# Kernel tuning notes

Measured on AMD Instinct MI355X. Metric: run time of the kernel, lower is better.

## Reference

```python
import jax, jax.numpy as jnp
import numpy as np

D_MODEL = 2048
N_HEADS = 32
N_KV_HEADS = 8
D_K = D_MODEL // N_HEADS          # 64
N_REP = N_HEADS // N_KV_HEADS     # 4
KV_DIM = N_KV_HEADS * D_K         # 512
B, T = 4, 2048


def setup_inputs() -> dict:
    key = jax.random.key(0)
    ks = jax.random.split(key, 9)
    s_in = 1.0 / np.sqrt(D_MODEL)
    x = jax.random.normal(ks[0], (B, T, D_MODEL), dtype=jnp.float32)
    Wq = jax.random.uniform(ks[1], (D_MODEL, D_MODEL), jnp.float32, -s_in, s_in)
    bq = jax.random.uniform(ks[2], (D_MODEL,), jnp.float32, -s_in, s_in)
    Wk = jax.random.uniform(ks[3], (D_MODEL, KV_DIM), jnp.float32, -s_in, s_in)
    bk = jax.random.uniform(ks[4], (KV_DIM,), jnp.float32, -s_in, s_in)
    Wv = jax.random.uniform(ks[5], (D_MODEL, KV_DIM), jnp.float32, -s_in, s_in)
    bv = jax.random.uniform(ks[6], (KV_DIM,), jnp.float32, -s_in, s_in)
    Wo = jax.random.uniform(ks[7], (D_MODEL, D_MODEL), jnp.float32, -s_in, s_in)
    bo = jax.random.uniform(ks[8], (D_MODEL,), jnp.float32, -s_in, s_in)
    return {"x": x, "Wq": Wq, "bq": bq, "Wk": Wk, "bk": bk,
            "Wv": Wv, "bv": bv, "Wo": Wo, "bo": bo}


def reference(x, Wq, bq, Wk, bk, Wv, bv, Wo, bo):
    Bsz, S, _ = x.shape
    # projections
    q = x @ Wq + bq                                   # (B, T, d_model)
    k = x @ Wk + bk                                   # (B, T, kv_dim)
    v = x @ Wv + bv
    # (B, n_kv, n_rep, T, d_k) for q; (B, n_kv, T, d_k) for k, v.
    # Grouping q by kv head avoids materializing repeated K/V.
    q = q.reshape(Bsz, S, N_KV_HEADS, N_REP, D_K).transpose(0, 2, 3, 1, 4)
    k = k.reshape(Bsz, S, N_KV_HEADS, D_K).transpose(0, 2, 1, 3)
    v = v.reshape(Bsz, S, N_KV_HEADS, D_K).transpose(0, 2, 1, 3)
    scale = 1.0 / np.sqrt(D_K).astype(np.float32)
    scores = jnp.einsum('bgrtd,bgsd->bgrts', q, k) * scale  # (B, n_kv, n_rep, T, T)
    causal = jnp.tril(jnp.ones((S, S), dtype=bool))
    scores = jnp.where(causal, scores, jnp.finfo(scores.dtype).min)
    p = jax.nn.softmax(scores, axis=-1)
    o = jnp.einsum('bgrts,bgsd->bgrtd', p, v)               # (B, n_kv, n_rep, T, d_k)
    o = o.transpose(0, 3, 1, 2, 4).reshape(Bsz, S, D_MODEL)
    return o @ Wo + bo
```

## Files before the change

kernel.cpp:

```cpp
#include <hip/hip_runtime.h>
#include <cstdint>
#include <cstddef>

typedef __attribute__((ext_vector_type(8))) short short8;
typedef __attribute__((ext_vector_type(4))) float f32x4;

#define D_MODEL 2048
#define KV_DIM  512
#define N_HEADS 32
#define N_KV    8
#define D_K     64
#define B_SZ    4
#define T_SEQ   2048
#define M_TOT   (B_SZ * T_SEQ)
#define N1      (D_MODEL + 2 * KV_DIM)
#define NEG_BIG (-1e30f)

__device__ __forceinline__ unsigned short f2bf(float f) {
    union { float f; unsigned int i; } c; c.f = f;
    unsigned int u = c.i;
    u += 0x7FFFu + ((u >> 16) & 1u);
    return (unsigned short)(u >> 16);
}

__device__ __forceinline__ unsigned int cvtpk_bf16(float lo, float hi) {
    unsigned int r;
    asm("v_cvt_pk_bf16_f32 %0, %1, %2" : "=v"(r) : "v"(lo), "v"(hi));
    return r;
}

__device__ __forceinline__ void async16(unsigned short* lds, const unsigned short* g) {
    __builtin_amdgcn_global_load_lds(
        (const __attribute__((address_space(1))) unsigned int*)g,
        (__attribute__((address_space(3))) unsigned int*)lds, 16, 0, 0);
}

__global__ __launch_bounds__(256)
void stage_x(const float* __restrict__ x, unsigned short* __restrict__ xb, int n) {
    for (int i = blockIdx.x * blockDim.x + threadIdx.x; i * 4 < n;
         i += gridDim.x * blockDim.x) {
        const f32x4 v = *(const f32x4*)&x[i * 4];
        unsigned short o[4];
#pragma unroll
        for (int k = 0; k < 4; k++) o[k] = f2bf(v[k]);
        *(uint64_t*)&xb[i * 4] = *(const uint64_t*)o;
    }
}

__global__ __launch_bounds__(256)
void transpose_f32_bf16(const float* __restrict__ src,
                        unsigned short* __restrict__ dst, int R, int C) {
    __shared__ unsigned short tile[32][34];
    int bx = blockIdx.x * 32;
    int by = blockIdx.y * 32;
    int tx = threadIdx.x;
    int ty = threadIdx.y;
#pragma unroll
    for (int i = 0; i < 32; i += 8)
        tile[ty + i][tx] = f2bf(src[(size_t)(by + ty + i) * C + bx + tx]);
    __syncthreads();
#pragma unroll
    for (int i = 0; i < 32; i += 8)
        dst[(size_t)(bx + ty + i) * R + by + tx] = tile[tx][ty + i];
}

template <int MODE>
__global__ __launch_bounds__(256)
void gemm_bt(const unsigned short* __restrict__ A,
             const unsigned short* __restrict__ Bt,
             const float* __restrict__ b0,
             const float* __restrict__ b1,
             const float* __restrict__ b2,
             unsigned short* __restrict__ out0,
             unsigned short* __restrict__ out1,
             unsigned short* __restrict__ out2,
             float* __restrict__ outF,
             int K) {
    __shared__ __align__(16) unsigned short As[128 * 32];
    __shared__ __align__(16) unsigned short Bs[128 * 32];

    const int t    = threadIdx.x;
    const int wave = t >> 6;
    const int lane = t & 63;
    const int quad = lane >> 4;
    const int l16  = lane & 15;
    const int wm   = (wave >> 1) * 64;
    const int wn   = (wave & 1) * 64;
    const int rowBase = blockIdx.y * 128;
    const int colBase = blockIdx.x * 128;

    f32x4 acc[4][4];
#pragma unroll
    for (int i = 0; i < 4; i++)
#pragma unroll
        for (int j = 0; j < 4; j++)
            acc[i][j] = (f32x4){0.f, 0.f, 0.f, 0.f};

    const int r0  = t >> 2;
    const int off = (t & 3) * 8;
    const unsigned short* Ap = A  + (size_t)(rowBase + r0) * K + off;
    const unsigned short* Bp = Bt + (size_t)(colBase + r0) * K + off;
    const size_t rowStep = (size_t)64 * K;

    for (int k0 = 0; k0 < K; k0 += 32) {
        *(short8*)&As[t * 8]         = *(const short8*)(Ap + k0);
        *(short8*)&As[(t + 256) * 8] = *(const short8*)(Ap + rowStep + k0);
        *(short8*)&Bs[t * 8]         = *(const short8*)(Bp + k0);
        *(short8*)&Bs[(t + 256) * 8] = *(const short8*)(Bp + rowStep + k0);
        __syncthreads();

        short8 af[4], bfr[4];
#pragma unroll
        for (int i = 0; i < 4; i++)
            af[i] = *(const short8*)&As[(wm + i * 16 + l16) * 32 + quad * 8];
#pragma unroll
        for (int i = 0; i < 4; i++)
            bfr[i] = *(const short8*)&Bs[(wn + i * 16 + l16) * 32 + quad * 8];

#pragma unroll
        for (int mi = 0; mi < 4; mi++)
#pragma unroll
            for (int ni = 0; ni < 4; ni++)
                acc[mi][ni] = __builtin_amdgcn_mfma_f32_16x16x32_bf16(
                    af[mi], bfr[ni], acc[mi][ni], 0, 0, 0);
        __syncthreads();
    }

#pragma unroll
    for (int mi = 0; mi < 4; mi++) {
        const int rowT = rowBase + wm + mi * 16 + quad * 4;
#pragma unroll
        for (int ni = 0; ni < 4; ni++) {
            const int col = colBase + wn + ni * 16 + l16;
#pragma unroll
            for (int r = 0; r < 4; r++) {
                float v = acc[mi][ni][r];
                const int rr = rowT + r;
                if (MODE == 0) {
                    if (col < D_MODEL) {
                        v += b0[col];
                        out0[(size_t)rr * D_MODEL + col] = f2bf(v);
                    } else if (col < D_MODEL + KV_DIM) {
                        const int c = col - D_MODEL;
                        v += b1[c];
                        out1[(size_t)rr * KV_DIM + c] = f2bf(v);
                    } else {
                        const int c = col - (D_MODEL + KV_DIM);
                        v += b2[c];
                        const int b   = rr >> 11;
                        const int tt  = rr & 2047;
                        const int kvh = c >> 6;
                        const int d   = c & 63;
                        out2[((size_t)((b * N_KV + kvh) * D_K + d)) * T_SEQ + tt] = f2bf(v);
                    }
                } else {
                    v += b0[col];
                    outF[(size_t)rr * D_MODEL + col] = v;
                }
            }
        }
    }
}

__global__ __launch_bounds__(256)
void attn_fwd(const unsigned short* __restrict__ qb,
              const unsigned short* __restrict__ kb,
              const unsigned short* __restrict__ vt,
              unsigned short* __restrict__ ob) {
    __shared__ __align__(16) unsigned short Ks[2][64 * 64];
    __shared__ __align__(16) unsigned short Vs[2][64 * 64];

    const int t    = threadIdx.x;
    const int wave = t >> 6;
    const int lane = t & 63;
    const int quad = lane >> 4;
    const int l16  = lane & 15;
    const int qt   = (int)gridDim.x - 1 - (int)blockIdx.x;
    const int h    = blockIdx.y;
    const int b    = blockIdx.z;
    const int kvh  = h >> 2;
    const int qBase = qt * 128;
    const int rowG  = b * T_SEQ;
    const size_t vtBase = (size_t)(b * N_KV + kvh) * D_K * T_SEQ;

    short8 qf[2][2];
#pragma unroll
    for (int mi = 0; mi < 2; mi++) {
        const int row = rowG + qBase + wave * 32 + mi * 16 + l16;
#pragma unroll
        for (int kk = 0; kk < 2; kk++)
            qf[mi][kk] = *(const short8*)&qb[(size_t)row * D_MODEL + h * D_K + kk * 32 + quad * 8];
    }

    f32x4 oacc[2][4];
#pragma unroll
    for (int i = 0; i < 2; i++)
#pragma unroll
        for (int j = 0; j < 4; j++)
            oacc[i][j] = (f32x4){0.f, 0.f, 0.f, 0.f};
    float m_run[2], l_run[2];
#pragma unroll
    for (int i = 0; i < 2; i++) { m_run[i] = NEG_BIG; l_run[i] = 0.f; }

    const int rr  = t >> 3;
    const int sc8 = ((t & 7) ^ (rr & 7)) << 3;

    auto stage = [&](int bi, int sB) {
#pragma unroll
        for (int i = 0; i < 2; i++) {
            const int row = i * 32 + rr;
            async16(&Ks[bi][(i * 32 + wave * 8) * 64],
                    kb + (size_t)(rowG + sB + row) * KV_DIM + kvh * D_K + sc8);
            async16(&Vs[bi][(i * 32 + wave * 8) * 64],
                    vt + vtBase + (size_t)row * T_SEQ + sB + sc8);
        }
    };

    const float scale = 0.125f;
    const int jMax = 2 * qt + 1;
    int buf = 0;

    stage(0, 0);
    __syncthreads();

    for (int j = 0; j <= jMax; ++j) {
        if (j < jMax) stage(buf ^ 1, (j + 1) * 64);

        if (!(j == jMax && wave < 2)) {
            const int sBase = j * 64;
            const bool diag = (j >= 2 * qt);
            const int sRel  = sBase - qBase;
            const char* KsB = (const char*)&Ks[buf][0];
            const char* VsB = (const char*)&Vs[buf][0];
            const int swz   = (l16 & 7) << 4;

            f32x4 sacc[4][2];
            __builtin_amdgcn_s_setprio(1);
#pragma unroll
            for (int ni = 0; ni < 4; ni++) {
                const int rowB = (ni * 16 + l16) * 128;
                const short8 kf0 = *(const short8*)(KsB + rowB + ((quad * 16) ^ swz));
                const short8 kf1 = *(const short8*)(KsB + rowB + ((64 + quad * 16) ^ swz));
#pragma unroll
                for (int mi = 0; mi < 2; mi++) {
                    f32x4 s = (f32x4){0.f, 0.f, 0.f, 0.f};
                    s = __builtin_amdgcn_mfma_f32_16x16x32_bf16(kf0, qf[mi][0], s, 0, 0, 0);
                    s = __builtin_amdgcn_mfma_f32_16x16x32_bf16(kf1, qf[mi][1], s, 0, 0, 0);
                    sacc[ni][mi] = s;
                }
            }
            __builtin_amdgcn_s_setprio(0);

            uint2 packed[4][2];
#pragma unroll
            for (int mi = 0; mi < 2; mi++) {
                float tm = NEG_BIG;
#pragma unroll
                for (int ni = 0; ni < 4; ni++)
#pragma unroll
                    for (int r = 0; r < 4; r++) {
                        float v = sacc[ni][mi][r] * scale;
                        if (diag) {
                            const int kc = sRel + ni * 16 + quad * 4 + r;
                            const int qr = wave * 32 + mi * 16 + l16;
                            if (kc > qr) v = NEG_BIG;
                        }
                        sacc[ni][mi][r] = v;
                        tm = fmaxf(tm, v);
                    }
                tm = fmaxf(tm, __shfl_xor(tm, 16));
                tm = fmaxf(tm, __shfl_xor(tm, 32));

                float mref = m_run[mi];
                float mnew, alpha;
                if (__all(tm <= mref + 8.f)) {
                    mnew = mref; alpha = 1.f;
                } else {
                    mnew  = fmaxf(mref, tm);
                    alpha = __expf(mref - mnew);
                    m_run[mi] = mnew;
#pragma unroll
                    for (int r2 = 0; r2 < 4; r2++) {
                        const float aR = __shfl(alpha, (lane & 48) + quad * 4 + r2);
#pragma unroll
                        for (int di = 0; di < 4; di++) oacc[mi][di][r2] *= aR;
                    }
                }
                float rs = 0.f;
#pragma unroll
                for (int ni = 0; ni < 4; ni++) {
#pragma unroll
                    for (int r = 0; r < 4; r++) {
                        const float p = __expf(sacc[ni][mi][r] - mnew);
                        sacc[ni][mi][r] = p;
                        rs += p;
                    }
                    packed[ni][mi].x = cvtpk_bf16(sacc[ni][mi][0], sacc[ni][mi][1]);
                    packed[ni][mi].y = cvtpk_bf16(sacc[ni][mi][2], sacc[ni][mi][3]);
                }
                rs += __shfl_xor(rs, 16);
                rs += __shfl_xor(rs, 32);
                l_run[mi] = l_run[mi] * alpha + rs;
            }

#pragma unroll
            for (int ks = 0; ks < 2; ks++) {
                short8 pa[2];
#pragma unroll
                for (int mi = 0; mi < 2; mi++) {
                    const int srcA = ((quad & 1) << 5) + l16;
                    const uint2 pL = packed[2 * ks][mi];
                    const uint2 pH = packed[2 * ks + 1][mi];
                    const unsigned a0x = __shfl((int)pL.x, srcA);
                    const unsigned a0y = __shfl((int)pL.y, srcA);
                    const unsigned b0x = __shfl((int)pL.x, srcA + 16);
                    const unsigned b0y = __shfl((int)pL.y, srcA + 16);
                    const unsigned a1x = __shfl((int)pH.x, srcA);
                    const unsigned a1y = __shfl((int)pH.y, srcA);
                    const unsigned b1x = __shfl((int)pH.x, srcA + 16);
                    const unsigned b1y = __shfl((int)pH.y, srcA + 16);
                    const int hi = quad >> 1;
                    union { unsigned u[4]; short8 s; } pw;
                    pw.u[0] = hi ? a1x : a0x;
                    pw.u[1] = hi ? a1y : a0y;
                    pw.u[2] = hi ? b1x : b0x;
                    pw.u[3] = hi ? b1y : b0y;
                    pa[mi] = pw.s;
                }
                __builtin_amdgcn_s_setprio(1);
#pragma unroll
                for (int di = 0; di < 4; di++) {
                    const short8 vb = *(const short8*)(VsB + (di * 16 + l16) * 128 +
                                                      ((ks * 64 + quad * 16) ^ swz));
#pragma unroll
                    for (int mi = 0; mi < 2; mi++)
                        oacc[mi][di] = __builtin_amdgcn_mfma_f32_16x16x32_bf16(
                            pa[mi], vb, oacc[mi][di], 0, 0, 0);
                }
                __builtin_amdgcn_s_setprio(0);
            }
        }

        __syncthreads();
        buf ^= 1;
    }

#pragma unroll
    for (int mi = 0; mi < 2; mi++) {
#pragma unroll
        for (int r = 0; r < 4; r++) {
            const float lr  = __shfl(l_run[mi], (lane & 48) + quad * 4 + r);
            const float inv = 1.f / lr;
            const int row = rowG + qBase + wave * 32 + mi * 16 + quad * 4 + r;
#pragma unroll
            for (int di = 0; di < 4; di++)
                ob[(size_t)row * D_MODEL + h * D_K + di * 16 + l16] =
                    f2bf(oacc[mi][di][r] * inv);
        }
    }
}

extern "C" void kernel_launch(void* const* d_in, const int* in_sizes, int n_in,
                              void* d_out, int out_size, void* d_ws, size_t ws_size,
                              hipStream_t stream) {
    const float* x  = (const float*)d_in[0];
    const float* Wq = (const float*)d_in[1];
    const float* bq = (const float*)d_in[2];
    const float* Wk = (const float*)d_in[3];
    const float* bk = (const float*)d_in[4];
    const float* Wv = (const float*)d_in[5];
    const float* bv = (const float*)d_in[6];
    const float* Wo = (const float*)d_in[7];
    const float* bo = (const float*)d_in[8];
    float* out = (float*)d_out;

    char* ws = (char*)d_ws;
    unsigned short* qb   = (unsigned short*)(ws);
    unsigned short* Wbuf = (unsigned short*)(ws + 33554432);
    unsigned short* xb   = (unsigned short*)(ws + 46137344);
    unsigned short* kb   = (unsigned short*)d_out;
    unsigned short* vt   = (unsigned short*)d_out + 4194304;

    stage_x<<<4096, 256, 0, stream>>>(x, xb, 16777216);

    dim3 tb(32, 8);
    transpose_f32_bf16<<<dim3(64, 64), tb, 0, stream>>>(Wq, Wbuf, 2048, 2048);
    transpose_f32_bf16<<<dim3(16, 64), tb, 0, stream>>>(Wk, Wbuf + 2048 * 2048, 2048, 512);
    transpose_f32_bf16<<<dim3(16, 64), tb, 0, stream>>>(Wv, Wbuf + 2560 * 2048, 2048, 512);

    gemm_bt<0><<<dim3(N1 / 128, M_TOT / 128), 256, 0, stream>>>(
        xb, Wbuf, bq, bk, bv, qb, kb, vt, nullptr, D_MODEL);

    transpose_f32_bf16<<<dim3(64, 64), tb, 0, stream>>>(Wo, Wbuf, 2048, 2048);

    attn_fwd<<<dim3(T_SEQ / 128, N_HEADS, B_SZ), 256, 0, stream>>>(qb, kb, vt, qb);

    gemm_bt<1><<<dim3(D_MODEL / 128, M_TOT / 128), 256, 0, stream>>>(
        qb, Wbuf, bo, nullptr, nullptr, nullptr, nullptr, nullptr, out, D_MODEL);
}
```

Before: 751.3 us.

## Load K/V fragments directly from global into registers, dropping LDS staging

Attention kernel no longer stages K and V tiles into double-buffered shared memory. Each wave loads its own K and V MFMA fragments straight from global memory into registers, prefetching the next tile's K after the QK^T MFMAs and the next V after the PV MFMAs. This removes the LDS round trip and the per-iteration block barrier. In exchange, each of the four waves fetches the same K/V data from global/L2 (four times the global traffic), and load latency is exposed unless the compiler overlaps it with the MFMAs.

```diff
diff --git a/kernel.cpp b/kernel.cpp
--- a/kernel.cpp
+++ b/kernel.cpp
@@ -27,12 +27,6 @@
     unsigned int r;
     asm("v_cvt_pk_bf16_f32 %0, %1, %2" : "=v"(r) : "v"(lo), "v"(hi));
     return r;
-}
-
-__device__ __forceinline__ void async16(unsigned short* lds, const unsigned short* g) {
-    __builtin_amdgcn_global_load_lds(
-        (const __attribute__((address_space(1))) unsigned int*)g,
-        (__attribute__((address_space(3))) unsigned int*)lds, 16, 0, 0);
 }
 
 __global__ __launch_bounds__(256)
@@ -167,9 +161,6 @@
               const unsigned short* __restrict__ kb,
               const unsigned short* __restrict__ vt,
               unsigned short* __restrict__ ob) {
-    __shared__ __align__(16) unsigned short Ks[2][64 * 64];
-    __shared__ __align__(16) unsigned short Vs[2][64 * 64];
-
     const int t    = threadIdx.x;
     const int wave = t >> 6;
     const int lane = t & 63;
@@ -181,7 +172,6 @@
     const int kvh  = h >> 2;
     const int qBase = qt * 128;
     const int rowG  = b * T_SEQ;
-    const size_t vtBase = (size_t)(b * N_KV + kvh) * D_K * T_SEQ;
 
     short8 qf[2][2];
 #pragma unroll
@@ -191,6 +181,23 @@
         for (int kk = 0; kk < 2; kk++)
             qf[mi][kk] = *(const short8*)&qb[(size_t)row * D_MODEL + h * D_K + kk * 32 + quad * 8];
     }
+
+    const unsigned short* kP = kb + (size_t)(rowG + l16) * KV_DIM + kvh * D_K + quad * 8;
+    const unsigned short* vP = vt + (size_t)((b * N_KV + kvh) * D_K + l16) * T_SEQ + quad * 8;
+
+    short8 kf[4][2];
+    short8 vf[4][2];
+
+#pragma unroll
+    for (int ni = 0; ni < 4; ni++)
+#pragma unroll
+        for (int kk = 0; kk < 2; kk++)
+            kf[ni][kk] = *(const short8*)(kP + (size_t)(ni * 16) * KV_DIM + kk * 32);
+#pragma unroll
+    for (int di = 0; di < 4; di++)
+#pragma unroll
+        for (int ks = 0; ks < 2; ks++)
+            vf[di][ks] = *(const short8*)(vP + (size_t)(di * 16) * T_SEQ + ks * 32);
 
     f32x4 oacc[2][4];
 #pragma unroll
@@ -202,56 +209,41 @@
 #pragma unroll
     for (int i = 0; i < 2; i++) { m_run[i] = NEG_BIG; l_run[i] = 0.f; }
 
-    const int rr  = t >> 3;
-    const int sc8 = ((t & 7) ^ (rr & 7)) << 3;
-
-    auto stage = [&](int bi, int sB) {
-#pragma unroll
-        for (int i = 0; i < 2; i++) {
-            const int row = i * 32 + rr;
-            async16(&Ks[bi][(i * 32 + wave * 8) * 64],
-                    kb + (size_t)(rowG + sB + row) * KV_DIM + kvh * D_K + sc8);
-            async16(&Vs[bi][(i * 32 + wave * 8) * 64],
-                    vt + vtBase + (size_t)row * T_SEQ + sB + sc8);
-        }
-    };
-
     const float scale = 0.125f;
     const int jMax = 2 * qt + 1;
-    int buf = 0;
-
-    stage(0, 0);
-    __syncthreads();
 
     for (int j = 0; j <= jMax; ++j) {
-        if (j < jMax) stage(buf ^ 1, (j + 1) * 64);
-
-        if (!(j == jMax && wave < 2)) {
-            const int sBase = j * 64;
-            const bool diag = (j >= 2 * qt);
-            const int sRel  = sBase - qBase;
-            const char* KsB = (const char*)&Ks[buf][0];
-            const char* VsB = (const char*)&Vs[buf][0];
-            const int swz   = (l16 & 7) << 4;
-
-            f32x4 sacc[4][2];
+        const bool skip = (j == jMax) && (wave < 2);
+        const bool diag = (j >= 2 * qt);
+        const int  sRel = j * 64 - qBase;
+
+        f32x4 sacc[4][2];
+        uint2 packed[4][2];
+
+        if (!skip) {
             __builtin_amdgcn_s_setprio(1);
 #pragma unroll
-            for (int ni = 0; ni < 4; ni++) {
-                const int rowB = (ni * 16 + l16) * 128;
-                const short8 kf0 = *(const short8*)(KsB + rowB + ((quad * 16) ^ swz));
-                const short8 kf1 = *(const short8*)(KsB + rowB + ((64 + quad * 16) ^ swz));
+            for (int ni = 0; ni < 4; ni++)
 #pragma unroll
                 for (int mi = 0; mi < 2; mi++) {
                     f32x4 s = (f32x4){0.f, 0.f, 0.f, 0.f};
-                    s = __builtin_amdgcn_mfma_f32_16x16x32_bf16(kf0, qf[mi][0], s, 0, 0, 0);
-                    s = __builtin_amdgcn_mfma_f32_16x16x32_bf16(kf1, qf[mi][1], s, 0, 0, 0);
+                    s = __builtin_amdgcn_mfma_f32_16x16x32_bf16(kf[ni][0], qf[mi][0], s, 0, 0, 0);
+                    s = __builtin_amdgcn_mfma_f32_16x16x32_bf16(kf[ni][1], qf[mi][1], s, 0, 0, 0);
                     sacc[ni][mi] = s;
                 }
-            }
             __builtin_amdgcn_s_setprio(0);
-
-            uint2 packed[4][2];
+        }
+
+        if (j < jMax) {
+            const int sB = (j + 1) * 64;
+#pragma unroll
+            for (int ni = 0; ni < 4; ni++)
+#pragma unroll
+                for (int kk = 0; kk < 2; kk++)
+                    kf[ni][kk] = *(const short8*)(kP + (size_t)(sB + ni * 16) * KV_DIM + kk * 32);
+        }
+
+        if (!skip) {
 #pragma unroll
             for (int mi = 0; mi < 2; mi++) {
                 float tm = NEG_BIG;
@@ -330,19 +322,23 @@
                 __builtin_amdgcn_s_setprio(1);
 #pragma unroll
                 for (int di = 0; di < 4; di++) {
-                    const short8 vb = *(const short8*)(VsB + (di * 16 + l16) * 128 +
-                                                      ((ks * 64 + quad * 16) ^ swz));
 #pragma unroll
                     for (int mi = 0; mi < 2; mi++)
                         oacc[mi][di] = __builtin_amdgcn_mfma_f32_16x16x32_bf16(
-                            pa[mi], vb, oacc[mi][di], 0, 0, 0);
+                            pa[mi], vf[di][ks], oacc[mi][di], 0, 0, 0);
                 }
                 __builtin_amdgcn_s_setprio(0);
             }
         }
 
-        __syncthreads();
-        buf ^= 1;
+        if (j < jMax) {
+            const int sB = (j + 1) * 64;
+#pragma unroll
+            for (int di = 0; di < 4; di++)
+#pragma unroll
+                for (int ks = 0; ks < 2; ks++)
+                    vf[di][ks] = *(const short8*)(vP + (size_t)(di * 16) * T_SEQ + sB + ks * 32);
+        }
     }
 
 #pragma unroll
```

After: 893.8 us. +19.0%, slower.

## Enlarge attention query tile to 256 rows with 8 waves and fold scale into Q

Applied to the files above, without the earlier changes.

The attention kernel now handles 256 query rows per block with 512 threads, so each staged K/V tile feeds twice as many waves and each thread issues one async load per tile. Per-wave causal skip and mask conditions replace the old diagonal logic. The softmax scale times log2(e) is folded into Q in the projection GEMM epilogue, so scores can go straight to the raw v_exp_f32 without a per-element multiply, and the max-update threshold is widened to match base 2. This trades fewer, larger blocks (lower occupancy, less load balancing) for more K/V reuse and fewer ALU ops. Rounding Q to bf16 after prescaling may shift numerics slightly.

```diff
diff --git a/kernel.cpp b/kernel.cpp
--- a/kernel.cpp
+++ b/kernel.cpp
@@ -15,6 +15,7 @@
 #define M_TOT   (B_SZ * T_SEQ)
 #define N1      (D_MODEL + 2 * KV_DIM)
 #define NEG_BIG (-1e30f)
+#define Q_PRESCALE 0.18033688011112042f
 
 __device__ __forceinline__ unsigned short f2bf(float f) {
     union { float f; unsigned int i; } c; c.f = f;
@@ -26,6 +27,12 @@
 __device__ __forceinline__ unsigned int cvtpk_bf16(float lo, float hi) {
     unsigned int r;
     asm("v_cvt_pk_bf16_f32 %0, %1, %2" : "=v"(r) : "v"(lo), "v"(hi));
+    return r;
+}
+
+__device__ __forceinline__ float e2(float x) {
+    float r;
+    asm("v_exp_f32 %0, %1" : "=v"(r) : "v"(x));
     return r;
 }
 
@@ -138,7 +145,7 @@
                 const int rr = rowT + r;
                 if (MODE == 0) {
                     if (col < D_MODEL) {
-                        v += b0[col];
+                        v = (v + b0[col]) * Q_PRESCALE;
                         out0[(size_t)rr * D_MODEL + col] = f2bf(v);
                     } else if (col < D_MODEL + KV_DIM) {
                         const int c = col - D_MODEL;
@@ -162,7 +169,7 @@
     }
 }
 
-__global__ __launch_bounds__(256)
+__global__ __launch_bounds__(512)
 void attn_fwd(const unsigned short* __restrict__ qb,
               const unsigned short* __restrict__ kb,
               const unsigned short* __restrict__ vt,
@@ -179,7 +186,7 @@
     const int h    = blockIdx.y;
     const int b    = blockIdx.z;
     const int kvh  = h >> 2;
-    const int qBase = qt * 128;
+    const int qBase = qt * 256;
     const int rowG  = b * T_SEQ;
     const size_t vtBase = (size_t)(b * N_KV + kvh) * D_K * T_SEQ;
 
@@ -206,18 +213,13 @@
     const int sc8 = ((t & 7) ^ (rr & 7)) << 3;
 
     auto stage = [&](int bi, int sB) {
-#pragma unroll
-        for (int i = 0; i < 2; i++) {
-            const int row = i * 32 + rr;
-            async16(&Ks[bi][(i * 32 + wave * 8) * 64],
-                    kb + (size_t)(rowG + sB + row) * KV_DIM + kvh * D_K + sc8);
-            async16(&Vs[bi][(i * 32 + wave * 8) * 64],
-                    vt + vtBase + (size_t)row * T_SEQ + sB + sc8);
-        }
+        async16(&Ks[bi][wave * 8 * 64],
+                kb + (size_t)(rowG + sB + rr) * KV_DIM + kvh * D_K + sc8);
+        async16(&Vs[bi][wave * 8 * 64],
+                vt + vtBase + (size_t)rr * T_SEQ + sB + sc8);
     };
 
-    const float scale = 0.125f;
-    const int jMax = 2 * qt + 1;
+    const int jMax = 4 * qt + 3;
     int buf = 0;
 
     stage(0, 0);
@@ -226,10 +228,11 @@
     for (int j = 0; j <= jMax; ++j) {
         if (j < jMax) stage(buf ^ 1, (j + 1) * 64);
 
-        if (!(j == jMax && wave < 2)) {
-            const int sBase = j * 64;
-            const bool diag = (j >= 2 * qt);
-            const int sRel  = sBase - qBase;
+        const int sRel = j * 64 - qBase;
+        const bool skip   = sRel > wave * 32 + 31;
+        const bool doMask = sRel + 63 > wave * 32;
+
+        if (!skip) {
             const char* KsB = (const char*)&Ks[buf][0];
             const char* VsB = (const char*)&Vs[buf][0];
             const int swz   = (l16 & 7) << 4;
@@ -259,8 +262,8 @@
                 for (int ni = 0; ni < 4; ni++)
 #pragma unroll
                     for (int r = 0; r < 4; r++) {
-                        float v = sacc[ni][mi][r] * scale;
-                        if (diag) {
+                        float v = sacc[ni][mi][r];
+                        if (doMask) {
                             const int kc = sRel + ni * 16 + quad * 4 + r;
                             const int qr = wave * 32 + mi * 16 + l16;
                             if (kc > qr) v = NEG_BIG;
@@ -273,11 +276,11 @@
 
                 float mref = m_run[mi];
                 float mnew, alpha;
-                if (__all(tm <= mref + 8.f)) {
+                if (__all(tm <= mref + 11.0f)) {
                     mnew = mref; alpha = 1.f;
                 } else {
                     mnew  = fmaxf(mref, tm);
-                    alpha = __expf(mref - mnew);
+                    alpha = e2(mref - mnew);
                     m_run[mi] = mnew;
 #pragma unroll
                     for (int r2 = 0; r2 < 4; r2++) {
@@ -291,7 +294,7 @@
                 for (int ni = 0; ni < 4; ni++) {
 #pragma unroll
                     for (int r = 0; r < 4; r++) {
-                        const float p = __expf(sacc[ni][mi][r] - mnew);
+                        const float p = e2(sacc[ni][mi][r] - mnew);
                         sacc[ni][mi][r] = p;
                         rs += p;
                     }
@@ -393,7 +396,7 @@
 
     transpose_f32_bf16<<<dim3(64, 64), tb, 0, stream>>>(Wo, Wbuf, 2048, 2048);
 
-    attn_fwd<<<dim3(T_SEQ / 128, N_HEADS, B_SZ), 256, 0, stream>>>(qb, kb, vt, qb);
+    attn_fwd<<<dim3(T_SEQ / 256, N_HEADS, B_SZ), 512, 0, stream>>>(qb, kb, vt, qb);
 
     gemm_bt<1><<<dim3(D_MODEL / 128, M_TOT / 128), 256, 0, stream>>>(
         qb, Wbuf, bo, nullptr, nullptr, nullptr, nullptr, nullptr, out, D_MODEL);
```

Result: no change. 751.4 us (+0.0%).
